# Optimization experiments

Hardware: AMD Instinct MI355X
Metric: run time of the kernel (lower is better)

## Reference

```python
import jax, jax.numpy as jnp
import numpy as np

NUM_HEADS = 8

def _heads(x, B, N, H):
    # [B, N, C] -> [B, H, N, d]
    return x.reshape(B, N, H, -1).transpose(0, 2, 1, 3)

def setup_inputs() -> dict:
    key = jax.random.key(0)
    k1, k2, k3, k4 = jax.random.split(key, 4)
    B, N, C = 8, 4096, 512
    x1 = jax.random.normal(k1, (B, N, C), dtype=jnp.float32)
    x2 = jax.random.normal(k2, (B, N, C), dtype=jnp.float32)
    # nn.Linear weights stored as [in, out] for x @ W
    Wkv1 = jax.random.normal(k3, (C, 2 * C), dtype=jnp.float32) * (C ** -0.5)
    Wkv2 = jax.random.normal(k4, (C, 2 * C), dtype=jnp.float32) * (C ** -0.5)
    return {"x1": x1, "x2": x2, "Wkv1": Wkv1, "Wkv2": Wkv2}

def reference(x1, x2, Wkv1, Wkv2):
    B, N, C = x1.shape
    H = NUM_HEADS
    d = C // H
    scale = d ** -0.5

    q1 = _heads(x1, B, N, H)                      # [B,H,N,d]
    q2 = _heads(x2, B, N, H)

    kv1 = (x1 @ Wkv1).reshape(B, N, 2, H, d).transpose(2, 0, 3, 1, 4)
    kv2 = (x2 @ Wkv2).reshape(B, N, 2, H, d).transpose(2, 0, 3, 1, 4)
    k1, v1 = kv1[0], kv1[1]                       # [B,H,N,d]
    k2, v2 = kv2[0], kv2[1]

    # contexts: K^T V over tokens -> small [B,H,d,d]
    ctx1 = jnp.einsum('bhnd,bhne->bhde', k1, v1) * scale
    ctx2 = jnp.einsum('bhnd,bhne->bhde', k2, v2) * scale

    # softmax over dim=-2 (the first d axis), then Q @ ctx
    a1 = jnp.einsum('bhnd,bhde->bhne', q1, jax.nn.softmax(ctx2, axis=-2))
    a2 = jnp.einsum('bhnd,bhde->bhne', q2, jax.nn.softmax(ctx1, axis=-2))

    out1 = a1.transpose(0, 2, 1, 3).reshape(B, N, C)
    out2 = a2.transpose(0, 2, 1, 3).reshape(B, N, C)
    return out1, out2
```

## Files before the change

kernel.cpp:

```cpp
#include <hip/hip_runtime.h>
#include <hip/hip_bf16.h>

typedef __bf16   bf16x8 __attribute__((ext_vector_type(8)));
typedef _Float16 f16x8  __attribute__((ext_vector_type(8)));
typedef _Float16 f16x4  __attribute__((ext_vector_type(4)));
typedef float    f32x4  __attribute__((ext_vector_type(4)));

#define NTOK 4096
#define CDIM 512
#define HEADS 8
#define HD 64

__device__ __forceinline__ void gload_lds16(const void* g, void* l) {
    __builtin_amdgcn_global_load_lds((const __attribute__((address_space(1))) void*)g,
                                     (__attribute__((address_space(3))) void*)l, 16, 0, 0);
}

__global__ __launch_bounds__(256, 4) void xpose_kernel(const float* __restrict__ x1,
                                                       const float* __restrict__ x2,
                                                       const float* __restrict__ Wkv1,
                                                       const float* __restrict__ Wkv2,
                                                       _Float16* __restrict__ xt,
                                                       _Float16* __restrict__ wvt) {
    const int t = threadIdx.x, w = t >> 6, l = t & 63;

    if (blockIdx.x >= 64) {
        if (blockIdx.z >= 8) return;
        const int s = blockIdx.x - 64;
        const float* W = (s ? Wkv2 : Wkv1);
        const int k0 = blockIdx.z * 64;
        const int j = blockIdx.y * 256 + w * 64 + l;

        f16x8 vh[8];
        #pragma unroll
        for (int q = 0; q < 64; ++q) {
            float v = W[(size_t)(k0 + q) * (2 * CDIM) + CDIM + j];
            vh[q >> 3][q & 7] = (_Float16)v;
        }
        _Float16* dh = wvt + ((size_t)s * CDIM + j) * CDIM + k0;
        #pragma unroll
        for (int q = 0; q < 8; ++q)
            *(f16x8*)&dh[q * 8] = vh[q];
        return;
    }

    const int kb = blockIdx.x, cb = blockIdx.y, sb = blockIdx.z;
    const int s = sb >> 3, b = sb & 7;
    const float* xs = (s ? x2 : x1) + (size_t)b * NTOK * CDIM
                    + (size_t)kb * 64 * CDIM + cb * 256;

    __shared__ _Float16 lds[64 * 256];

    float4 v[16];
    #pragma unroll
    for (int i = 0; i < 16; ++i) {
        const int n = 4 * i + w;
        v[i] = *(const float4*)&xs[(size_t)n * CDIM + l * 4];
    }
    #pragma unroll
    for (int i = 0; i < 16; ++i) {
        const int n = 4 * i + w;
        f16x4 p = {(_Float16)v[i].x, (_Float16)v[i].y, (_Float16)v[i].z, (_Float16)v[i].w};
        *(f16x4*)&lds[n * 256 + ((l ^ (n >> 3)) << 2)] = p;
    }
    __syncthreads();

    const int kk8 = (l & 7);
    _Float16* dst = xt + ((size_t)(sb * 64 + kb) * CDIM + cb * 256) * 64;
    #pragma unroll
    for (int q = 0; q < 8; ++q) {
        const int cw = 64 * w + 8 * q + (l >> 3);
        const int c4s = (cw >> 2) ^ kk8, c2 = cw & 3;
        const int base = (c4s << 2) + c2 + kk8 * 8 * 256;
        f16x8 o;
        #pragma unroll
        for (int j = 0; j < 8; ++j)
            o[j] = lds[base + j * 256];
        *(f16x8*)&dst[(size_t)cw * 64 + kk8 * 8] = o;
    }
}

__global__ __launch_bounds__(256) void gram_kernel(const _Float16* __restrict__ xt,
                                                   _Float16* __restrict__ GPh) {
    const int id = blockIdx.x;
    const int vid = (id & 7) * 64 + (id >> 3);
    const int sb = vid >> 5, rest = vid & 31;
    const int split = rest >> 4, tile = rest & 15;
    const int I0 = (tile >> 2) * 128, J0 = (tile & 3) * 128;
    const _Float16* xb = xt + (size_t)sb * CDIM * NTOK;

    __shared__ _Float16 Ih[2][128 * 64];
    __shared__ _Float16 Jh[2][128 * 64];

    const int t = threadIdx.x, w = t >> 6, l = t & 63;
    const int wm = w >> 1, wn = w & 1, l15 = l & 15, lk = l >> 4;
    const int colr = w * 8 + (l >> 3), pos = l & 7;

    f32x4 acc[4][4];
    #pragma unroll
    for (int f = 0; f < 4; ++f)
        #pragma unroll
        for (int g = 0; g < 4; ++g) acc[f][g] = (f32x4)(0.0f);

    auto STAGE = [&](int bufi, int it) {
        const _Float16* kb = xb + (size_t)(split * 32 + it) * CDIM * 64;
        #pragma unroll
        for (int r = 0; r < 4; ++r) {
            const int colw = r * 32 + colr;
            const int swz = ((pos ^ (colw & 7)) << 3);
            gload_lds16(kb + (size_t)(I0 + colw) * 64 + swz, &Ih[bufi][r * 2048 + w * 512]);
            gload_lds16(kb + (size_t)(J0 + colw) * 64 + swz, &Jh[bufi][r * 2048 + w * 512]);
        }
    };

    STAGE(0, 0);
    for (int it = 0; it < 32; ++it) {
        const int cur = it & 1;
        if (it < 31) {
            STAGE(cur ^ 1, it + 1);
            asm volatile("s_waitcnt vmcnt(8)" ::: "memory");
        } else {
            asm volatile("s_waitcnt vmcnt(0)" ::: "memory");
        }
        __builtin_amdgcn_s_barrier();

        const _Float16* Ib = &Ih[cur][0];
        const _Float16* Jb = &Jh[cur][0];
        __builtin_amdgcn_s_setprio(1);
        #pragma unroll
        for (int ks = 0; ks < 2; ++ks) {
            f16x8 a[4], bb[4];
            #pragma unroll
            for (int f = 0; f < 4; ++f) {
                const int i = wm * 64 + f * 16 + l15;
                a[f] = *(const f16x8*)&Ib[i * 64 + ((ks * 4 + lk) ^ (i & 7)) * 8];
            }
            #pragma unroll
            for (int g = 0; g < 4; ++g) {
                const int j = wn * 64 + g * 16 + l15;
                bb[g] = *(const f16x8*)&Jb[j * 64 + ((ks * 4 + lk) ^ (j & 7)) * 8];
            }
            #pragma unroll
            for (int f = 0; f < 4; ++f)
                #pragma unroll
                for (int g = 0; g < 4; ++g)
                    acc[f][g] = __builtin_amdgcn_mfma_f32_16x16x32_f16(a[f], bb[g], acc[f][g], 0, 0, 0);
        }
        __builtin_amdgcn_s_setprio(0);
        __builtin_amdgcn_s_barrier();
    }

    _Float16* Gout = GPh + ((size_t)split * 16 + sb) * CDIM * CDIM;
    #pragma unroll
    for (int f = 0; f < 4; ++f)
        #pragma unroll
        for (int g = 0; g < 4; ++g) {
            const int row0 = I0 + wm * 64 + f * 16 + lk * 4;
            const int col  = J0 + wn * 64 + g * 16 + l15;
            #pragma unroll
            for (int r = 0; r < 4; ++r)
                Gout[(size_t)(row0 + r) * CDIM + col] = (_Float16)acc[f][g][r];
        }
}

__global__ __launch_bounds__(256) void t_kernel(const _Float16* __restrict__ GPh,
                                                const _Float16* __restrict__ wvt,
                                                _Float16* __restrict__ TP) {
    const int id = blockIdx.x;
    const int vid = (id & 7) * 64 + (id >> 3);
    const int sb = vid >> 5, rest = vid & 31;
    const int ks2 = rest >> 4, tile = rest & 15;
    const int s = sb >> 3;
    const int I0 = (tile >> 2) * 128, J0 = (tile & 3) * 128;
    const _Float16* G0 = GPh + (size_t)sb * CDIM * CDIM;
    const _Float16* G1 = GPh + ((size_t)16 + sb) * CDIM * CDIM;
    const _Float16* Bv = wvt + (size_t)s * CDIM * CDIM;

    __shared__ _Float16 Ah[128 * 64];
    __shared__ _Float16 Jh[128 * 64];

    const int t = threadIdx.x, w = t >> 6, l = t & 63;
    const int wm = w >> 1, wn = w & 1, l15 = l & 15, lk = l >> 4;
    const int colr = w * 8 + (l >> 3), pos = l & 7;

    f32x4 acc[4][4];
    #pragma unroll
    for (int f = 0; f < 4; ++f)
        #pragma unroll
        for (int g = 0; g < 4; ++g) acc[f][g] = (f32x4)(0.0f);

    for (int it = 0; it < 4; ++it) {
        const int k0 = ks2 * 256 + it * 64;
        __syncthreads();
        #pragma unroll
        for (int r = 0; r < 4; ++r) {
            const int col = r * 32 + colr;
            const int swz = ((pos ^ (col & 7)) << 3);
            gload_lds16(Bv + (size_t)(J0 + col) * CDIM + k0 + swz, &Jh[r * 2048 + w * 512]);
        }
        #pragma unroll
        for (int r = 0; r < 4; ++r) {
            const int i = r * 32 + (t >> 3), ch = t & 7;
            const size_t off = (size_t)(I0 + i) * CDIM + k0 + ch * 8;
            f16x8 a0 = *(const f16x8*)&G0[off];
            f16x8 a1 = *(const f16x8*)&G1[off];
            f16x8 sum = a0 + a1;
            *(f16x8*)&Ah[i * 64 + ((ch ^ (i & 7)) << 3)] = sum;
        }
        __syncthreads();
        __builtin_amdgcn_s_setprio(1);
        #pragma unroll
        for (int ks = 0; ks < 2; ++ks) {
            f16x8 a[4], bb[4];
            #pragma unroll
            for (int f = 0; f < 4; ++f) {
                const int i = wm * 64 + f * 16 + l15;
                a[f] = *(const f16x8*)&Ah[i * 64 + ((ks * 4 + lk) ^ (i & 7)) * 8];
            }
            #pragma unroll
            for (int g = 0; g < 4; ++g) {
                const int j = wn * 64 + g * 16 + l15;
                bb[g] = *(const f16x8*)&Jh[j * 64 + ((ks * 4 + lk) ^ (j & 7)) * 8];
            }
            #pragma unroll
            for (int f = 0; f < 4; ++f)
                #pragma unroll
                for (int g = 0; g < 4; ++g)
                    acc[f][g] = __builtin_amdgcn_mfma_f32_16x16x32_f16(a[f], bb[g], acc[f][g], 0, 0, 0);
        }
        __builtin_amdgcn_s_setprio(0);
    }

    _Float16* Tb = TP + ((size_t)ks2 * 16 + sb) * CDIM * CDIM;
    #pragma unroll
    for (int f = 0; f < 4; ++f)
        #pragma unroll
        for (int g = 0; g < 4; ++g) {
            const int row0 = I0 + wm * 64 + f * 16 + lk * 4;
            const int col  = J0 + wn * 64 + g * 16 + l15;
            #pragma unroll
            for (int r = 0; r < 4; ++r)
                Tb[(size_t)(row0 + r) * CDIM + col] = (_Float16)acc[f][g][r];
        }
}

__global__ __launch_bounds__(256) void ctx_gemm_kernel(const _Float16* __restrict__ TP,
                                                       const float* __restrict__ Wkv1,
                                                       const float* __restrict__ Wkv2,
                                                       float* __restrict__ CP) {
    const int h = blockIdx.x, sb = blockIdx.y, kq = blockIdx.z;
    const int s = sb >> 3;
    const float* W  = (s == 0 ? Wkv1 : Wkv2);
    const _Float16* T0 = TP + (size_t)sb * CDIM * CDIM;
    const _Float16* T1 = TP + ((size_t)16 + sb) * CDIM * CDIM;

    __shared__ float Kt[64][65];
    __shared__ float Tt[64][65];

    const int t = threadIdx.x;
    const int td = t >> 4, te = t & 15;
    float acc[4][4] = {};

    for (int it = 0; it < 2; ++it) {
        const int kc = kq * 128 + it * 64;
        __syncthreads();
        for (int i = 0; i < 16; ++i) {
            const int idx = t + i * 256;
            const int r = idx >> 6, cc = idx & 63;
            Kt[r][cc] = W[(size_t)(kc + r) * (2 * CDIM) + h * HD + cc];
            Tt[r][cc] = (float)T0[(size_t)(kc + r) * CDIM + h * HD + cc]
                      + (float)T1[(size_t)(kc + r) * CDIM + h * HD + cc];
        }
        __syncthreads();
        for (int k = 0; k < 64; ++k) {
            float a[4], bb[4];
            #pragma unroll
            for (int i = 0; i < 4; ++i) a[i] = Kt[k][td * 4 + i];
            #pragma unroll
            for (int j = 0; j < 4; ++j) bb[j] = Tt[k][te * 4 + j];
            #pragma unroll
            for (int i = 0; i < 4; ++i)
                #pragma unroll
                for (int j = 0; j < 4; ++j) acc[i][j] += a[i] * bb[j];
        }
    }
    float* out = CP + (size_t)(((kq * 16 + sb) * HEADS) + h) * HD * HD;
    for (int i = 0; i < 4; ++i)
        for (int j = 0; j < 4; ++j)
            out[(size_t)(td * 4 + i) * HD + te * 4 + j] = acc[i][j];
}

__global__ __launch_bounds__(256) void ctx_fin_kernel(const float* __restrict__ CP,
                                                      _Float16* __restrict__ smT) {
    const int h = blockIdx.x, sb = blockIdx.y;

    __shared__ float ctxs[64][65];
    __shared__ float mred[64], sred[64];

    const int t = threadIdx.x;
    const float scale = 0.125f;
    #pragma unroll
    for (int i = 0; i < 4; ++i) {
        const int idx4 = t + i * 256;
        const int d = idx4 >> 4, e4 = idx4 & 15;
        f32x4 sum = (f32x4)(0.0f);
        #pragma unroll
        for (int kq = 0; kq < 4; ++kq) {
            const float* p = CP + (size_t)(((kq * 16 + sb) * HEADS) + h) * HD * HD;
            f32x4 v = *(const f32x4*)&p[d * HD + e4 * 4];
            sum += v;
        }
        *(f32x4*)&ctxs[d][e4 * 4] = sum * scale;
    }
    __syncthreads();
    if (t < 64) {
        float m = -1e30f;
        for (int d = 0; d < 64; ++d) m = fmaxf(m, ctxs[d][t]);
        float ssum = 0.f;
        for (int d = 0; d < 64; ++d) ssum += expf(ctxs[d][t] - m);
        mred[t] = m;
        sred[t] = 1.0f / ssum;
    }
    __syncthreads();
    _Float16* smout = smT + (size_t)(sb * HEADS + h) * HD * HD;
    #pragma unroll
    for (int i = 0; i < 16; ++i) {
        const int idx = t + i * 256;
        const int e = idx >> 6, d = idx & 63;
        smout[e * HD + d] = (_Float16)(expf(ctxs[d][e] - mred[e]) * sred[e]);
    }
}

__global__ __launch_bounds__(256) void out_kernel(const float* __restrict__ x1,
                                                  const float* __restrict__ x2,
                                                  const _Float16* __restrict__ smT,
                                                  float* __restrict__ out) {
    const int id = blockIdx.x;
    const int vid = (id & 7) * 512 + (id >> 3);
    const int h = vid & 7, nt = (vid >> 3) & 31, sb = vid >> 8;
    const int s = sb >> 3, b = sb & 7;
    const float* xs = (s ? x2 : x1) + (size_t)b * NTOK * CDIM;
    const _Float16* sm = smT + (size_t)((((1 - s) * 8 + b) * HEADS) + h) * HD * HD;
    const int n0 = nt * 128;

    __shared__ _Float16 Axt[128 * 64];
    __shared__ _Float16 Bsm[64 * 64];

    const int t = threadIdx.x, w = t >> 6, l = t & 63;
    const int l15 = l & 15, lk = l >> 4;

    #pragma unroll
    for (int r = 0; r < 2; ++r) {
        const int e = r * 32 + w * 8 + (l >> 3), pos = l & 7;
        gload_lds16(sm + (size_t)e * HD + ((pos ^ (e & 7)) << 3), &Bsm[r * 2048 + w * 512]);
    }
    #pragma unroll
    for (int p = 0; p < 8; ++p) {
        const int row = p * 16 + (t >> 4), f4c = t & 15;
        float4 u = *(const float4*)&xs[(size_t)(n0 + row) * CDIM + h * HD + f4c * 4];
        f16x4 q = {(_Float16)u.x, (_Float16)u.y, (_Float16)u.z, (_Float16)u.w};
        const int byte = row * 128 + (((f4c >> 1) ^ (row & 7)) << 4) + ((f4c & 1) << 3);
        *(f16x4*)((char*)Axt + byte) = q;
    }
    __syncthreads();

    f32x4 acc[2][4];
    #pragma unroll
    for (int m = 0; m < 2; ++m)
        #pragma unroll
        for (int g = 0; g < 4; ++g) acc[m][g] = (f32x4)(0.0f);

    #pragma unroll
    for (int ks = 0; ks < 2; ++ks) {
        f16x8 a[2], bb[4];
        #pragma unroll
        for (int m = 0; m < 2; ++m) {
            const int row = w * 32 + m * 16 + l15;
            a[m] = *(const f16x8*)((char*)Axt + row * 128 + (((ks * 4 + lk) ^ (row & 7)) << 4));
        }
        #pragma unroll
        for (int g = 0; g < 4; ++g) {
            const int e = g * 16 + l15;
            bb[g] = *(const f16x8*)((char*)Bsm + e * 128 + (((ks * 4 + lk) ^ (e & 7)) << 4));
        }
        #pragma unroll
        for (int m = 0; m < 2; ++m)
            #pragma unroll
            for (int g = 0; g < 4; ++g)
                acc[m][g] = __builtin_amdgcn_mfma_f32_16x16x32_f16(a[m], bb[g], acc[m][g], 0, 0, 0);
    }

    float* ob = out + (size_t)s * (8ULL * NTOK * CDIM) + (size_t)b * NTOK * CDIM;
    #pragma unroll
    for (int m = 0; m < 2; ++m)
        #pragma unroll
        for (int g = 0; g < 4; ++g) {
            const int row0 = n0 + w * 32 + m * 16 + lk * 4;
            const int col  = h * HD + g * 16 + l15;
            #pragma unroll
            for (int r = 0; r < 4; ++r)
                ob[(size_t)(row0 + r) * CDIM + col] = acc[m][g][r];
        }
}

extern "C" void kernel_launch(void* const* d_in, const int* in_sizes, int n_in,
                              void* d_out, int out_size, void* d_ws, size_t ws_size,
                              hipStream_t stream) {
    const float* x1   = (const float*)d_in[0];
    const float* x2   = (const float*)d_in[1];
    const float* Wkv1 = (const float*)d_in[2];
    const float* Wkv2 = (const float*)d_in[3];
    float* out = (float*)d_out;

    char* base = (char*)d_out;
    _Float16* XT   = (_Float16*)(base + 0);
    _Float16* WVT  = (_Float16*)(base + 67108864);
    _Float16* GPh  = (_Float16*)(base + 68157440);
    _Float16* TP   = (_Float16*)(base + 84934656);
    float*    CP   = (float*)(base + 101711872);
    _Float16* SMT  = (_Float16*)d_ws;

    hipLaunchKernelGGL(xpose_kernel, dim3(66, 2, 16), dim3(256), 0, stream,
                       x1, x2, Wkv1, Wkv2, XT, WVT);
    hipLaunchKernelGGL(gram_kernel, dim3(512), dim3(256), 0, stream, XT, GPh);
    hipLaunchKernelGGL(t_kernel, dim3(512), dim3(256), 0, stream, GPh, WVT, TP);
    hipLaunchKernelGGL(ctx_gemm_kernel, dim3(8, 16, 4), dim3(256), 0, stream,
                       TP, Wkv1, Wkv2, CP);
    hipLaunchKernelGGL(ctx_fin_kernel, dim3(8, 16), dim3(256), 0, stream, CP, SMT);
    hipLaunchKernelGGL(out_kernel, dim3(4096), dim3(256), 0, stream, x1, x2, SMT, out);
}
```

Measured before the change: 151.7 us.

## Enlarge gram tiles to 256x256 with 512 threads and 4-way K split

The Gram kernel moves from 128x128 tiles with 256 threads and a 2-way token split to 256x256 tiles with 512 threads (8 waves) and a 4-way token split, each wave computing 128x64 in two half-passes with extra barriers. The larger tiles raise arithmetic intensity per LDS byte staged and halve the block count. In exchange, t_kernel must now read and sum four fp16 partial Gram matrices instead of two, which adds memory traffic and extra fp16 rounding, and the workspace offsets are shifted to fit the larger partial buffer. LDS use doubles to 128KB per block, which limits occupancy.

```diff
diff --git a/kernel.cpp b/kernel.cpp
--- a/kernel.cpp
+++ b/kernel.cpp
@@ -80,43 +80,47 @@
     }
 }
 
-__global__ __launch_bounds__(256) void gram_kernel(const _Float16* __restrict__ xt,
-                                                   _Float16* __restrict__ GPh) {
+__global__ __launch_bounds__(512, 2) void gram_kernel(const _Float16* __restrict__ xt,
+                                                      float* __restrict__ ,
+                                                      _Float16* __restrict__ GPh) {
     const int id = blockIdx.x;
-    const int vid = (id & 7) * 64 + (id >> 3);
-    const int sb = vid >> 5, rest = vid & 31;
-    const int split = rest >> 4, tile = rest & 15;
-    const int I0 = (tile >> 2) * 128, J0 = (tile & 3) * 128;
+    const int vid = (id & 7) * 32 + (id >> 3);
+    const int sb = vid >> 4, rest = vid & 15;
+    const int split = rest >> 2, tile = rest & 3;
+    const int I0 = (tile >> 1) * 256, J0 = (tile & 1) * 256;
     const _Float16* xb = xt + (size_t)sb * CDIM * NTOK;
 
-    __shared__ _Float16 Ih[2][128 * 64];
-    __shared__ _Float16 Jh[2][128 * 64];
+    __shared__ _Float16 Atile[2][256 * 64];
+    __shared__ _Float16 Btile[2][256 * 64];
 
     const int t = threadIdx.x, w = t >> 6, l = t & 63;
-    const int wm = w >> 1, wn = w & 1, l15 = l & 15, lk = l >> 4;
-    const int colr = w * 8 + (l >> 3), pos = l & 7;
-
-    f32x4 acc[4][4];
-    #pragma unroll
-    for (int f = 0; f < 4; ++f)
+    const int wm = w >> 2, wn = w & 3;
+    const int l15 = l & 15, lk = l >> 4;
+    const int scol = w * 8 + (l >> 3), spos = l & 7;
+
+    f32x4 acc[8][4];
+    #pragma unroll
+    for (int f = 0; f < 8; ++f)
         #pragma unroll
         for (int g = 0; g < 4; ++g) acc[f][g] = (f32x4)(0.0f);
 
     auto STAGE = [&](int bufi, int it) {
-        const _Float16* kb = xb + (size_t)(split * 32 + it) * CDIM * 64;
+        const _Float16* kbase = xb + (size_t)(split * 16 + it) * (CDIM * 64);
         #pragma unroll
         for (int r = 0; r < 4; ++r) {
-            const int colw = r * 32 + colr;
-            const int swz = ((pos ^ (colw & 7)) << 3);
-            gload_lds16(kb + (size_t)(I0 + colw) * 64 + swz, &Ih[bufi][r * 2048 + w * 512]);
-            gload_lds16(kb + (size_t)(J0 + colw) * 64 + swz, &Jh[bufi][r * 2048 + w * 512]);
+            const int col = r * 64 + scol;
+            const int swz = ((spos ^ (col & 7)) << 3);
+            gload_lds16(kbase + (size_t)(I0 + col) * 64 + swz,
+                        &Atile[bufi][(r * 64 + w * 8) * 64]);
+            gload_lds16(kbase + (size_t)(J0 + col) * 64 + swz,
+                        &Btile[bufi][(r * 64 + w * 8) * 64]);
         }
     };
 
     STAGE(0, 0);
-    for (int it = 0; it < 32; ++it) {
+    for (int it = 0; it < 16; ++it) {
         const int cur = it & 1;
-        if (it < 31) {
+        if (it < 15) {
             STAGE(cur ^ 1, it + 1);
             asm volatile("s_waitcnt vmcnt(8)" ::: "memory");
         } else {
@@ -124,38 +128,53 @@
         }
         __builtin_amdgcn_s_barrier();
 
-        const _Float16* Ib = &Ih[cur][0];
-        const _Float16* Jb = &Jh[cur][0];
-        __builtin_amdgcn_s_setprio(1);
+        const _Float16* Ab = &Atile[cur][0];
+        const _Float16* Bb = &Btile[cur][0];
+
         #pragma unroll
         for (int ks = 0; ks < 2; ++ks) {
-            f16x8 a[4], bb[4];
-            #pragma unroll
-            for (int f = 0; f < 4; ++f) {
-                const int i = wm * 64 + f * 16 + l15;
-                a[f] = *(const f16x8*)&Ib[i * 64 + ((ks * 4 + lk) ^ (i & 7)) * 8];
-            }
+            f16x8 bfr[4], afr[4];
             #pragma unroll
             for (int g = 0; g < 4; ++g) {
                 const int j = wn * 64 + g * 16 + l15;
-                bb[g] = *(const f16x8*)&Jb[j * 64 + ((ks * 4 + lk) ^ (j & 7)) * 8];
+                bfr[g] = *(const f16x8*)&Bb[j * 64 + ((ks * 4 + lk) ^ (j & 7)) * 8];
             }
             #pragma unroll
-            for (int f = 0; f < 4; ++f)
+            for (int q = 0; q < 4; ++q) {
+                const int i = wm * 128 + q * 16 + l15;
+                afr[q] = *(const f16x8*)&Ab[i * 64 + ((ks * 4 + lk) ^ (i & 7)) * 8];
+            }
+            __builtin_amdgcn_s_setprio(1);
+            #pragma unroll
+            for (int q = 0; q < 4; ++q)
                 #pragma unroll
                 for (int g = 0; g < 4; ++g)
-                    acc[f][g] = __builtin_amdgcn_mfma_f32_16x16x32_f16(a[f], bb[g], acc[f][g], 0, 0, 0);
-        }
-        __builtin_amdgcn_s_setprio(0);
-        __builtin_amdgcn_s_barrier();
+                    acc[q][g] = __builtin_amdgcn_mfma_f32_16x16x32_f16(afr[q], bfr[g], acc[q][g], 0, 0, 0);
+            __builtin_amdgcn_s_setprio(0);
+            __builtin_amdgcn_s_barrier();
+
+            #pragma unroll
+            for (int q = 0; q < 4; ++q) {
+                const int i = wm * 128 + (q + 4) * 16 + l15;
+                afr[q] = *(const f16x8*)&Ab[i * 64 + ((ks * 4 + lk) ^ (i & 7)) * 8];
+            }
+            __builtin_amdgcn_s_setprio(1);
+            #pragma unroll
+            for (int q = 0; q < 4; ++q)
+                #pragma unroll
+                for (int g = 0; g < 4; ++g)
+                    acc[q + 4][g] = __builtin_amdgcn_mfma_f32_16x16x32_f16(afr[q], bfr[g], acc[q + 4][g], 0, 0, 0);
+            __builtin_amdgcn_s_setprio(0);
+            __builtin_amdgcn_s_barrier();
+        }
     }
 
     _Float16* Gout = GPh + ((size_t)split * 16 + sb) * CDIM * CDIM;
     #pragma unroll
-    for (int f = 0; f < 4; ++f)
+    for (int f = 0; f < 8; ++f)
         #pragma unroll
         for (int g = 0; g < 4; ++g) {
-            const int row0 = I0 + wm * 64 + f * 16 + lk * 4;
+            const int row0 = I0 + wm * 128 + f * 16 + lk * 4;
             const int col  = J0 + wn * 64 + g * 16 + l15;
             #pragma unroll
             for (int r = 0; r < 4; ++r)
@@ -174,6 +193,8 @@
     const int I0 = (tile >> 2) * 128, J0 = (tile & 3) * 128;
     const _Float16* G0 = GPh + (size_t)sb * CDIM * CDIM;
     const _Float16* G1 = GPh + ((size_t)16 + sb) * CDIM * CDIM;
+    const _Float16* G2 = GPh + ((size_t)32 + sb) * CDIM * CDIM;
+    const _Float16* G3 = GPh + ((size_t)48 + sb) * CDIM * CDIM;
     const _Float16* Bv = wvt + (size_t)s * CDIM * CDIM;
 
     __shared__ _Float16 Ah[128 * 64];
@@ -204,7 +225,9 @@
             const size_t off = (size_t)(I0 + i) * CDIM + k0 + ch * 8;
             f16x8 a0 = *(const f16x8*)&G0[off];
             f16x8 a1 = *(const f16x8*)&G1[off];
-            f16x8 sum = a0 + a1;
+            f16x8 a2 = *(const f16x8*)&G2[off];
+            f16x8 a3 = *(const f16x8*)&G3[off];
+            f16x8 sum = (a0 + a1) + (a2 + a3);
             *(f16x8*)&Ah[i * 64 + ((ch ^ (i & 7)) << 3)] = sum;
         }
         __syncthreads();
@@ -416,13 +439,13 @@
     _Float16* XT   = (_Float16*)(base + 0);
     _Float16* WVT  = (_Float16*)(base + 67108864);
     _Float16* GPh  = (_Float16*)(base + 68157440);
-    _Float16* TP   = (_Float16*)(base + 84934656);
-    float*    CP   = (float*)(base + 101711872);
+    _Float16* TP   = (_Float16*)(base + 101711872);
+    float*    CP   = (float*)(base + 118489088);
     _Float16* SMT  = (_Float16*)d_ws;
 
     hipLaunchKernelGGL(xpose_kernel, dim3(66, 2, 16), dim3(256), 0, stream,
                        x1, x2, Wkv1, Wkv2, XT, WVT);
-    hipLaunchKernelGGL(gram_kernel, dim3(512), dim3(256), 0, stream, XT, GPh);
+    hipLaunchKernelGGL(gram_kernel, dim3(256), dim3(512), 0, stream, XT, (float*)nullptr, GPh);
     hipLaunchKernelGGL(t_kernel, dim3(512), dim3(256), 0, stream, GPh, WVT, TP);
     hipLaunchKernelGGL(ctx_gemm_kernel, dim3(8, 16, 4), dim3(256), 0, stream,
                        TP, Wkv1, Wkv2, CP);
```

After: 155.9 us. 1.03x slower.
